# Kernel optimization log

Hardware: AMD Instinct MI355X
Metric: run time of the kernel (lower is better)

The kernel has to match this reference:

```python
import jax, jax.numpy as jnp
import numpy as np

N_NODES = 100000
N_EDGES = 1600000
D_IN = 128
D_HID = 128
D_EMB = 128
D_OUT = 16


def _glorot(key, shape):
    fan_in, fan_out = shape
    lim = (6.0 / (fan_in + fan_out)) ** 0.5
    return jax.random.uniform(key, shape, jnp.float32, -lim, lim)


def setup_inputs() -> dict:
    key = jax.random.key(0)
    ks = jax.random.split(key, 12)
    x = jax.random.normal(ks[0], (N_NODES, D_IN), jnp.float32)
    edge_index = jax.random.randint(ks[1], (2, N_EDGES), 0, N_NODES, jnp.int32)
    return {
        "x": x,
        "edge_index": edge_index,
        # SAGEConv layer 0: neighbor weight, self(root) weight, bias
        "Wn0": _glorot(ks[2], (D_IN, D_HID)),
        "Ws0": _glorot(ks[3], (D_IN, D_HID)),
        "b0": jnp.zeros((D_HID,), jnp.float32),
        # SAGEConv layer 1
        "Wn1": _glorot(ks[4], (D_HID, D_HID)),
        "Ws1": _glorot(ks[5], (D_HID, D_HID)),
        "b1": jnp.zeros((D_HID,), jnp.float32),
        # SAGEConv layer 2 (to embedding dim)
        "Wn2": _glorot(ks[6], (D_HID, D_EMB)),
        "Ws2": _glorot(ks[7], (D_HID, D_EMB)),
        "b2": jnp.zeros((D_EMB,), jnp.float32),
        # final fc
        "Wfc": _glorot(ks[8], (D_EMB, D_OUT)),
        "bfc": jnp.zeros((D_OUT,), jnp.float32),
    }


def _sage_conv(x, src, dst, deg_inv, Wn, Ws, b):
    # mean-aggregate source features at destination nodes, then transform.
    agg = jax.ops.segment_sum(x[src], dst, num_segments=N_NODES)  # [N, d]
    mean = agg * deg_inv[:, None]
    return mean @ Wn + x @ Ws + b


def reference(x, edge_index, Wn0, Ws0, b0, Wn1, Ws1, b1, Wn2, Ws2, b2, Wfc, bfc):
    src, dst = edge_index[0], edge_index[1]
    deg = jax.ops.segment_sum(jnp.ones((src.shape[0],), x.dtype), dst,
                              num_segments=N_NODES)
    deg_inv = 1.0 / jnp.maximum(deg, 1.0)

    h = _sage_conv(x, src, dst, deg_inv, Wn0, Ws0, b0)
    h = jax.nn.relu(h)  # dropout omitted (eval mode / deterministic reference)
    h = _sage_conv(h, src, dst, deg_inv, Wn1, Ws1, b1)
    h = jax.nn.relu(h)
    emb = _sage_conv(h, src, dst, deg_inv, Wn2, Ws2, b2)
    y = emb @ Wfc + bfc
    return emb, jax.nn.log_softmax(y, axis=1)
```

## Files before the change

### kernel.cpp

```cpp
#include <hip/hip_runtime.h>
#include <hip/hip_fp16.h>

#define NN 100000
#define NE 1600000
#define DD 128
#define CAP 64
#define FRAG_ELEMS 16384

typedef __attribute__((ext_vector_type(8))) _Float16 half8;
typedef __attribute__((ext_vector_type(4))) float f32x4;

__global__ void k_xcast(const float* __restrict__ x, _Float16* __restrict__ xh) {
    int t = blockIdx.x * 256 + threadIdx.x;
    const float* p = x + (size_t)t * 8;
    float4 v0 = *(const float4*)p;
    float4 v1 = *(const float4*)(p + 4);
    half8 o = { (_Float16)v0.x, (_Float16)v0.y, (_Float16)v0.z, (_Float16)v0.w,
                (_Float16)v1.x, (_Float16)v1.y, (_Float16)v1.z, (_Float16)v1.w };
    *(half8*)(xh + (size_t)t * 8) = o;
}

__global__ void k_fill(const int* __restrict__ src, const int* __restrict__ dst,
                       int* __restrict__ cnt, int* __restrict__ bkt) {
    int e = blockIdx.x * 256 + threadIdx.x;
    if (e < NE) {
        int d = dst[e];
        int p = atomicAdd(&cnt[d], 1);
        if (p < CAP) bkt[(size_t)d * CAP + p] = src[e];
    }
}

__global__ __launch_bounds__(256) void k_wprep(const float* __restrict__ W0,
                                               const float* __restrict__ W1,
                                               const float* __restrict__ W2,
                                               const float* __restrict__ W3,
                                               const float* __restrict__ W4,
                                               const float* __restrict__ W5,
                                               _Float16* __restrict__ out) {
    int mat = blockIdx.x >> 6;
    int e = (blockIdx.x & 63) * 256 + threadIdx.x;
    const float* W = (mat == 0) ? W0 : (mat == 1) ? W1 : (mat == 2) ? W2
                   : (mat == 3) ? W3 : (mat == 4) ? W4 : W5;
    int j = e & 7;
    int lane = (e >> 3) & 63;
    int ct = (e >> 9) & 7;
    int kt = e >> 12;
    int k = kt * 32 + (lane >> 4) * 8 + j;
    int n = ct * 16 + (lane & 15);
    float v = W[k * 128 + n];
    _Float16 hi = (_Float16)v;
    _Float16 lo = (_Float16)(v - (float)hi);
    _Float16* mb = out + (size_t)mat * 2 * FRAG_ELEMS;
    mb[e] = hi;
    mb[FRAG_ELEMS + e] = lo;
}

__global__ __launch_bounds__(256) void k_agg(const _Float16* __restrict__ h,
                                             const int* __restrict__ cnt,
                                             const int* __restrict__ bkt,
                                             _Float16* __restrict__ mean) {
    int node = blockIdx.x * 4 + (threadIdx.x >> 6);
    if (node >= NN) return;
    int lane = threadIdx.x & 63;
    int q = lane >> 4;
    int col = (lane & 15) * 8;
    int deg = cnt[node];
    int n = deg > CAP ? CAP : deg;
    const int* b = bkt + (size_t)node * CAP;
    float a[8] = {};
    int i = 0;
    for (; i + 8 <= n; i += 8) {
        int s0 = b[i + q];
        int s1 = b[i + 4 + q];
        half8 v0 = *(const half8*)(h + (size_t)s0 * DD + col);
        half8 v1 = *(const half8*)(h + (size_t)s1 * DD + col);
#pragma unroll
        for (int j = 0; j < 8; ++j) a[j] += (float)v0[j] + (float)v1[j];
    }
    if (i + 4 <= n) {
        int s0 = b[i + q];
        half8 v0 = *(const half8*)(h + (size_t)s0 * DD + col);
#pragma unroll
        for (int j = 0; j < 8; ++j) a[j] += (float)v0[j];
        i += 4;
    }
    if (i + q < n) {
        int s = b[i + q];
        half8 v = *(const half8*)(h + (size_t)s * DD + col);
#pragma unroll
        for (int j = 0; j < 8; ++j) a[j] += (float)v[j];
    }
#pragma unroll
    for (int j = 0; j < 8; ++j) {
        a[j] += __shfl_xor(a[j], 16);
        a[j] += __shfl_xor(a[j], 32);
    }
    if (q == 0) {
        float di = 1.0f / (float)(deg > 1 ? deg : 1);
        half8 o;
#pragma unroll
        for (int j = 0; j < 8; ++j) o[j] = (_Float16)(a[j] * di);
        *(half8*)(mean + (size_t)node * DD + col) = o;
    }
}

__global__ __launch_bounds__(256) void k_gemm(
    const _Float16* __restrict__ meanp, const _Float16* __restrict__ hin,
    const _Float16* __restrict__ wf,
    const float* __restrict__ bias,
    _Float16* __restrict__ outh, float* __restrict__ outf) {

    int t = threadIdx.x;
    int wave = t >> 6;
    int lane = t & 63;
    int m16 = lane & 15;
    int kg = lane >> 4;
    int rowA = blockIdx.x * 64 + wave * 16 + m16;
    if (rowA >= NN) rowA = NN - 1;

    f32x4 acc[8] = {};

#pragma unroll
    for (int s = 0; s < 2; ++s) {
        const _Float16* Whi = wf + s * 2 * FRAG_ELEMS;
        const _Float16* Wlo = Whi + FRAG_ELEMS;
        const _Float16* Ap = (s ? hin : meanp) + (size_t)rowA * DD;
#pragma unroll
        for (int kt = 0; kt < 4; ++kt) {
            half8 a = *(const half8*)(Ap + kt * 32 + kg * 8);
#pragma unroll
            for (int ct = 0; ct < 8; ++ct) {
                int off = ((kt * 8 + ct) * 64 + lane) * 8;
                half8 bh = *(const half8*)(Whi + off);
                half8 bl = *(const half8*)(Wlo + off);
                acc[ct] = __builtin_amdgcn_mfma_f32_16x16x32_f16(a, bh, acc[ct], 0, 0, 0);
                acc[ct] = __builtin_amdgcn_mfma_f32_16x16x32_f16(a, bl, acc[ct], 0, 0, 0);
            }
        }
    }

    int rbase = blockIdx.x * 64 + wave * 16 + kg * 4;
    if (outh) {
#pragma unroll
        for (int ct = 0; ct < 8; ++ct) {
            int col = ct * 16 + m16;
            float bv = bias[col];
#pragma unroll
            for (int i = 0; i < 4; ++i) {
                int r = rbase + i;
                if (r < NN)
                    outh[(size_t)r * DD + col] = (_Float16)fmaxf(acc[ct][i] + bv, 0.0f);
            }
        }
    } else {
#pragma unroll
        for (int ct = 0; ct < 8; ++ct) {
            int col = ct * 16 + m16;
            float bv = bias[col];
#pragma unroll
            for (int i = 0; i < 4; ++i) {
                int r = rbase + i;
                if (r < NN)
                    outf[(size_t)r * DD + col] = acc[ct][i] + bv;
            }
        }
    }
}

__global__ __launch_bounds__(256) void k_fc(const float* __restrict__ emb,
                                            const float* __restrict__ Wfc,
                                            const float* __restrict__ bfc,
                                            float* __restrict__ out) {
    __shared__ float se[16 * 128];
    __shared__ float swt[128 * 16];
    int t = threadIdx.x;
    int nb = blockIdx.x * 16;
    int idx = t * 8;
    *(float4*)(se + idx)      = *(const float4*)(emb + (size_t)nb * 128 + idx);
    *(float4*)(se + idx + 4)  = *(const float4*)(emb + (size_t)nb * 128 + idx + 4);
    *(float4*)(swt + idx)     = *(const float4*)(Wfc + idx);
    *(float4*)(swt + idx + 4) = *(const float4*)(Wfc + idx + 4);
    __syncthreads();

    int nl = t >> 4;
    int o = t & 15;
    float acc = bfc[o];
    const float* er = se + nl * 128;
#pragma unroll 8
    for (int k = 0; k < 128; ++k)
        acc += er[k] * swt[k * 16 + o];

    float m = acc;
#pragma unroll
    for (int d = 1; d < 16; d <<= 1) m = fmaxf(m, __shfl_xor(m, d, 16));
    float e = expf(acc - m);
    float ssum = e;
#pragma unroll
    for (int d = 1; d < 16; d <<= 1) ssum += __shfl_xor(ssum, d, 16);
    out[(size_t)(nb + nl) * 16 + o] = (acc - m) - logf(ssum);
}

extern "C" void kernel_launch(void* const* d_in, const int* in_sizes, int n_in,
                              void* d_out, int out_size, void* d_ws, size_t ws_size,
                              hipStream_t stream) {
    const float* x   = (const float*)d_in[0];
    const int*   ei  = (const int*)d_in[1];
    const float* Wn0 = (const float*)d_in[2];
    const float* Ws0 = (const float*)d_in[3];
    const float* b0  = (const float*)d_in[4];
    const float* Wn1 = (const float*)d_in[5];
    const float* Ws1 = (const float*)d_in[6];
    const float* b1  = (const float*)d_in[7];
    const float* Wn2 = (const float*)d_in[8];
    const float* Ws2 = (const float*)d_in[9];
    const float* b2  = (const float*)d_in[10];
    const float* Wfc = (const float*)d_in[11];
    const float* bfc = (const float*)d_in[12];

    const int* src = ei;
    const int* dst = ei + NE;

    float* emb_out = (float*)d_out;
    float* lsm_out = emb_out + (size_t)NN * 128;

    char* ws = (char*)d_ws;
    _Float16* xh    = (_Float16*)(ws);
    _Float16* hA    = (_Float16*)(ws + 25600000);
    _Float16* hB    = (_Float16*)(ws + 51200000);
    _Float16* mean  = (_Float16*)(ws + 76800000);
    int*      cnt   = (int*)     (ws + 102400000);
    int*      bkt   = (int*)     (ws + 102800000);
    _Float16* wfrag = (_Float16*)(ws + 128400000);

    hipMemsetAsync(cnt, 0, NN * sizeof(int), stream);
    k_xcast<<<(NN * DD / 8) / 256, 256, 0, stream>>>(x, xh);
    k_wprep<<<384, 256, 0, stream>>>(Wn0, Ws0, Wn1, Ws1, Wn2, Ws2, wfrag);
    k_fill<<<(NE + 255) / 256, 256, 0, stream>>>(src, dst, cnt, bkt);

    const int agg_blocks  = (NN + 3) / 4;
    const int gemm_blocks = (NN + 63) / 64;
    _Float16* wf0 = wfrag;
    _Float16* wf1 = wfrag + 4 * FRAG_ELEMS;
    _Float16* wf2 = wfrag + 8 * FRAG_ELEMS;

    k_agg<<<agg_blocks, 256, 0, stream>>>(xh, cnt, bkt, mean);
    k_gemm<<<gemm_blocks, 256, 0, stream>>>(mean, xh, wf0, b0, hA, nullptr);

    k_agg<<<agg_blocks, 256, 0, stream>>>(hA, cnt, bkt, mean);
    k_gemm<<<gemm_blocks, 256, 0, stream>>>(mean, hA, wf1, b1, hB, nullptr);

    k_agg<<<agg_blocks, 256, 0, stream>>>(hB, cnt, bkt, mean);
    k_gemm<<<gemm_blocks, 256, 0, stream>>>(mean, hB, wf2, b2, nullptr, emb_out);

    k_fc<<<NN / 16, 256, 0, stream>>>(emb_out, Wfc, bfc, lsm_out);
}
```

Measured before the change: 574.5 us.

## Build CSR buckets via atomicExch linked lists instead of atomicAdd scatter

Replaces the atomicAdd-based bucket fill with a two-pass approach. First, each edge is pushed onto a per-destination linked list using atomicExch on a head array, which is initialised inside the cast kernel so the memset is no longer needed. Then one thread per node walks its list and writes the bucket contiguously along with the count. The goal is to cut scattered atomic/store traffic to the bucket array, but the list walk is a serial, latency-bound pointer chase per node, and bucket order differs from before.

```diff
diff --git a/kernel.cpp b/kernel.cpp
--- a/kernel.cpp
+++ b/kernel.cpp
@@ -9,9 +9,12 @@
 
 typedef __attribute__((ext_vector_type(8))) _Float16 half8;
 typedef __attribute__((ext_vector_type(4))) float f32x4;
-
-__global__ void k_xcast(const float* __restrict__ x, _Float16* __restrict__ xh) {
+typedef __attribute__((ext_vector_type(4))) int intv4;
+
+__global__ void k_xcast(const float* __restrict__ x, _Float16* __restrict__ xh,
+                        int* __restrict__ head) {
     int t = blockIdx.x * 256 + threadIdx.x;
+    if (t < NN) head[t] = -1;
     const float* p = x + (size_t)t * 8;
     float4 v0 = *(const float4*)p;
     float4 v1 = *(const float4*)(p + 4);
@@ -20,14 +23,41 @@
     *(half8*)(xh + (size_t)t * 8) = o;
 }
 
-__global__ void k_fill(const int* __restrict__ src, const int* __restrict__ dst,
-                       int* __restrict__ cnt, int* __restrict__ bkt) {
-    int e = blockIdx.x * 256 + threadIdx.x;
-    if (e < NE) {
-        int d = dst[e];
-        int p = atomicAdd(&cnt[d], 1);
-        if (p < CAP) bkt[(size_t)d * CAP + p] = src[e];
-    }
+__global__ __launch_bounds__(256) void k_link(const int* __restrict__ src,
+                                              const int* __restrict__ dst,
+                                              int* __restrict__ head,
+                                              int* __restrict__ link) {
+    int t = blockIdx.x * 256 + threadIdx.x;
+    if (t >= NE / 4) return;
+    intv4 d = ((const intv4*)dst)[t];
+    intv4 s = ((const intv4*)src)[t];
+    int e0 = t * 4;
+    int o0 = atomicExch(&head[d.x], e0);
+    int o1 = atomicExch(&head[d.y], e0 + 1);
+    int o2 = atomicExch(&head[d.z], e0 + 2);
+    int o3 = atomicExch(&head[d.w], e0 + 3);
+    intv4 w0 = { o0, s.x, o1, s.y };
+    intv4 w1 = { o2, s.z, o3, s.w };
+    ((intv4*)link)[t * 2]     = w0;
+    ((intv4*)link)[t * 2 + 1] = w1;
+}
+
+__global__ __launch_bounds__(256) void k_flat(const int* __restrict__ head,
+                                              const int* __restrict__ link,
+                                              int* __restrict__ cnt,
+                                              int* __restrict__ bkt) {
+    int d = blockIdx.x * 256 + threadIdx.x;
+    if (d >= NN) return;
+    int cur = head[d];
+    int p = 0;
+    int* b = bkt + (size_t)d * CAP;
+    while (cur >= 0) {
+        int2 l = *(const int2*)(link + (size_t)cur * 2);
+        if (p < CAP) b[p] = l.y;
+        ++p;
+        cur = l.x;
+    }
+    cnt[d] = p;
 }
 
 __global__ __launch_bounds__(256) void k_wprep(const float* __restrict__ W0,
@@ -232,10 +262,13 @@
     int*      bkt   = (int*)     (ws + 102800000);
     _Float16* wfrag = (_Float16*)(ws + 128400000);
 
-    hipMemsetAsync(cnt, 0, NN * sizeof(int), stream);
-    k_xcast<<<(NN * DD / 8) / 256, 256, 0, stream>>>(x, xh);
+    int* link = (int*)(ws + 76800000);
+    int* head = (int*)(ws + 76800000 + 12800000);
+
+    k_xcast<<<(NN * DD / 8) / 256, 256, 0, stream>>>(x, xh, head);
     k_wprep<<<384, 256, 0, stream>>>(Wn0, Ws0, Wn1, Ws1, Wn2, Ws2, wfrag);
-    k_fill<<<(NE + 255) / 256, 256, 0, stream>>>(src, dst, cnt, bkt);
+    k_link<<<(NE / 4 + 255) / 256, 256, 0, stream>>>(src, dst, head, link);
+    k_flat<<<(NN + 255) / 256, 256, 0, stream>>>(head, link, cnt, bkt);
 
     const int agg_blocks  = (NN + 3) / 4;
     const int gemm_blocks = (NN + 63) / 64;
```

Measured after the change: 579.9 us. About the same (+0.9%).
